# Performance work log

Measured on AMD Instinct MI355X. Metric: run time of the kernel, lower is better.

## Reference

```python
import jax, jax.numpy as jnp
import numpy as np

B, S, H, D, HID = 2, 4096, 16, 64, 1024
NUM_HASHES, CHUNK, NUM_BUCKETS = 2, 64, 128
N_BEFORE, N_AFTER = 1, 0
HASH_SEED = 0
SELF_MASK_VALUE = -1e5  # fp32 self-mask value from source buffers
EPS = 1e-6


def _look_adjacent(x, n_before, n_after):
    # x: [B,H,C,chunk,...]; concat chunks rolled along chunk axis (2) onto within-chunk axis (3)
    slices = [jnp.roll(x, -i, axis=2) for i in range(-n_before, n_after + 1)]
    return jnp.concatenate(slices, axis=3)


def _hash_vectors(vectors, rotations, num_buckets):
    # vectors: [B,H,S,D]; rotations: [H,D,NUM_HASHES,num_buckets//2] (shared q/k, seed reset in source)
    v = jax.lax.stop_gradient(vectors)  # vectors.detach() in source
    rotated = jnp.einsum('bhsd,hdnr->bhnsr', v, rotations)
    rotated = jnp.concatenate([rotated, -rotated], axis=-1)
    buckets = jnp.argmax(rotated, axis=-1)  # [B,H,NUM_HASHES,S]
    offsets = (jnp.arange(NUM_HASHES) * num_buckets).reshape(1, 1, -1, 1)
    return (buckets + offsets).reshape(vectors.shape[0], H, -1)  # [B,H,NUM_HASHES*S]


def _sorted_and_undo(buckets, seq_len):
    orig = jnp.arange(NUM_HASHES * seq_len) % seq_len
    scaled = seq_len * buckets + orig  # stable within-bucket ordering by position
    sorted_idx = jnp.argsort(scaled, axis=-1)
    undo_idx = jnp.argsort(sorted_idx, axis=-1)  # scatter-inverse of the sort
    return sorted_idx, undo_idx


def _len_and_dim_norm(x):
    var = jnp.mean(x * x, axis=-1, keepdims=True)
    return x * jax.lax.rsqrt(var + EPS) * np.float32(1.0 / np.sqrt(D))


def setup_inputs() -> dict:
    key = jax.random.key(0)
    k1, k2, k3, k4 = jax.random.split(key, 4)
    return {
        'decoder_states': jax.random.normal(k1, (B, S, HID), jnp.float32),
        'hidden_states': jax.random.normal(k2, (B, S, HID), jnp.float32),
        'w_qk': jax.random.normal(k3, (HID, H * D), jnp.float32) / np.float32(np.sqrt(HID)),
        'w_v': jax.random.normal(k4, (HID, H * D), jnp.float32) / np.float32(np.sqrt(HID)),
    }


def reference(decoder_states, hidden_states, w_qk, w_v):
    # projections (bias-free, Reformer-style), split heads -> [B,H,S,D]
    q = (decoder_states @ w_qk).reshape(B, S, H, D).transpose(0, 2, 1, 3)
    k = (hidden_states @ w_qk).reshape(B, S, H, D).transpose(0, 2, 1, 3)
    v = (hidden_states @ w_v).reshape(B, S, H, D).transpose(0, 2, 1, 3)

    rotations = jax.random.normal(jax.random.key(HASH_SEED),
                                  (H, D, NUM_HASHES, NUM_BUCKETS // 2), jnp.float32)
    q_buckets = _hash_vectors(q, rotations, NUM_BUCKETS)
    k_buckets = _hash_vectors(k, rotations, NUM_BUCKETS)
    sorted_q_idx, _ = _sorted_and_undo(q_buckets, S)
    sorted_k_idx, undo_k_idx = _sorted_and_undo(k_buckets, S)
    sorted_q_pos = sorted_q_idx % S
    sorted_k_pos = sorted_k_idx % S

    gather = lambda x, idx: jnp.take_along_axis(x, idx[..., None], axis=2)
    qs = gather(q, sorted_q_pos)  # [B,H,NUM_HASHES*S,D]
    ks = gather(k, sorted_k_pos)
    vs = gather(v, sorted_k_pos)

    n_chunks = NUM_HASHES * S // CHUNK
    to_chunks = lambda x: x.reshape(B, H, n_chunks, CHUNK, D)
    qs, ks, vs = to_chunks(qs), to_chunks(ks), to_chunks(vs)
    ks = _len_and_dim_norm(ks)

    ks = _look_adjacent(ks, N_BEFORE, N_AFTER)  # [B,H,C,2*CHUNK,D]
    vs = _look_adjacent(vs, N_BEFORE, N_AFTER)
    dots = jnp.einsum('bhcqd,bhckd->bhcqk', qs, ks)

    # self-mask: query position == adjacent key position (both from sorted QUERY idx, per source)
    q_idx = sorted_q_pos.reshape(B, H, n_chunks, CHUNK)
    kv_idx = _look_adjacent(q_idx, N_BEFORE, N_AFTER)  # [B,H,C,2*CHUNK]
    self_mask = q_idx[..., :, None] != kv_idx[..., None, :]
    dots = jnp.where(self_mask, dots, SELF_MASK_VALUE)

    logits = jax.nn.logsumexp(dots, axis=-1, keepdims=True)
    probs = jnp.exp(dots - logits)
    out = jnp.einsum('bhcqk,bhckd->bhcqd', probs, vs)

    out = out.reshape(B, H, NUM_HASHES * S, D)
    logits = logits.reshape(B, H, NUM_HASHES * S)
    # ReverseSort uses the KEY undo indices (as in source)
    out = jnp.take_along_axis(out, undo_k_idx[..., None], axis=2)
    logits = jnp.take_along_axis(logits, undo_k_idx, axis=2)

    # merge hash rounds via logsumexp weights (num_hashes > 1 branch)
    out = out.reshape(B, H, NUM_HASHES, S, D)
    logits = logits.reshape(B, H, NUM_HASHES, S, 1)
    w = jnp.exp(logits - jax.nn.logsumexp(logits, axis=2, keepdims=True))
    out = jnp.sum(out * w, axis=2)  # [B,H,S,D]
    return out.transpose(0, 2, 1, 3).reshape(B, S, H * D)
```

## Files before the change

kernel.cpp:

```cpp
#include <hip/hip_runtime.h>
#include <cstdint>
#include <cstddef>

#define BB 2
#define SS 4096
#define HH 16
#define DD 64
#define HID 1024
#define NHASH 2
#define CHUNK 64
#define NBUCK 128
#define NCHUNKS 128
#define NSORT 8192
#define BHN 32

#define KC_BLOCK 288

static constexpr size_t SZ_QKV  = (size_t)BB*HH*SS*DD*4;
static constexpr size_t OFF_Q   = 0;
static constexpr size_t OFF_K   = OFF_Q + SZ_QKV;
static constexpr size_t OFF_V   = OFF_K + SZ_QKV;
static constexpr size_t OFF_ROT = OFF_V + SZ_QKV;
static constexpr size_t OFF_QB  = OFF_ROT + (size_t)131072*4;
static constexpr size_t OFF_KB  = OFF_QB + (size_t)BHN*NSORT*4;
static constexpr size_t OFF_SQ  = OFF_KB + (size_t)BHN*NSORT*4;
static constexpr size_t OFF_SK  = OFF_SQ + (size_t)BHN*NSORT*4;
static constexpr size_t OFF_OUTR= OFF_SK + (size_t)BHN*NSORT*4;
static constexpr size_t OFF_LR  = OFF_OUTR + (size_t)BHN*NSORT*DD*4;
static constexpr size_t OFF_QBF = OFF_LR + (size_t)BHN*NSORT*4;
static constexpr size_t OFF_KBF = OFF_QBF + (size_t)BHN*SS*DD*2;
static constexpr size_t WS_REQUIRED = OFF_KBF + (size_t)BHN*SS*DD*2;

__device__ __forceinline__ float nofma_mul(float a, float b) {
  float r = a * b;
  asm("" : "+v"(r));
  return r;
}

__device__ __forceinline__ float xla_log1p_f32(float x) {
  float t = nofma_mul(-0.5f, x) + 1.0f;
  float small = nofma_mul(t, x);
  float onep = 1.0f + x;
  float big = (float)log((double)onep);
  return (fabsf(x) < 1e-4f) ? small : big;
}

__device__ __forceinline__ float erfinv_xla_f32(float x) {
  float nxx = -nofma_mul(x, x);
  float w = -xla_log1p_f32(nxx);
  float p;
  if (w < 5.0f) {
    float ww = w - 2.5f;
    p = 2.81022636e-08f;
    p = nofma_mul(p, ww) + 3.43273939e-07f;
    p = nofma_mul(p, ww) + -3.5233877e-06f;
    p = nofma_mul(p, ww) + -4.39150654e-06f;
    p = nofma_mul(p, ww) + 0.00021858087f;
    p = nofma_mul(p, ww) + -0.00125372503f;
    p = nofma_mul(p, ww) + -0.00417768164f;
    p = nofma_mul(p, ww) + 0.246640727f;
    p = nofma_mul(p, ww) + 1.50140941f;
  } else {
    float ww = sqrtf(w) - 3.0f;
    p = -0.000200214257f;
    p = nofma_mul(p, ww) + 0.000100950558f;
    p = nofma_mul(p, ww) + 0.00134934322f;
    p = nofma_mul(p, ww) + -0.00367342844f;
    p = nofma_mul(p, ww) + 0.00573950773f;
    p = nofma_mul(p, ww) + -0.0076224613f;
    p = nofma_mul(p, ww) + 0.00943887047f;
    p = nofma_mul(p, ww) + 1.00167406f;
    p = nofma_mul(p, ww) + 2.83297682f;
  }
  return nofma_mul(p, x);
}

__global__ void gen_rot_kernel(float* __restrict__ rot) {
  unsigned i = blockIdx.x * 256 + threadIdx.x;
  if (i >= 131072u) return;
  unsigned x0 = 0u, x1 = i;
  const unsigned ks2 = 0x1BD11BDAu;
#define TF_ROUND(r) { x0 += x1; x1 = (x1 << r) | (x1 >> (32 - r)); x1 ^= x0; }
  TF_ROUND(13) TF_ROUND(15) TF_ROUND(26) TF_ROUND(6)
              x1 += ks2 + 1u;
  TF_ROUND(17) TF_ROUND(29) TF_ROUND(16) TF_ROUND(24)
   x0 += ks2; x1 += 2u;
  TF_ROUND(13) TF_ROUND(15) TF_ROUND(26) TF_ROUND(6)
              x1 += 3u;
  TF_ROUND(17) TF_ROUND(29) TF_ROUND(16) TF_ROUND(24)
              x1 += ks2 + 4u;
  TF_ROUND(13) TF_ROUND(15) TF_ROUND(26) TF_ROUND(6)
   x0 += ks2; x1 += 5u;
#undef TF_ROUND
  unsigned bits = x0 ^ x1;
  float f = __uint_as_float(0x3f800000u | (bits >> 9)) - 1.0f;
  float u = f * 2.0f - 0.99999994f;
  u = fmaxf(-0.99999994f, u);
  rot[i] = nofma_mul(1.41421356f, erfinv_xla_f32(u));
}

__device__ __forceinline__ unsigned short f2bf(float f) {
  unsigned u = __float_as_uint(f);
  return (unsigned short)((u + 0x7fffu + ((u >> 16) & 1u)) >> 16);
}

__global__ __launch_bounds__(256) void gemm_kernel(const float* __restrict__ A,
                                                   const float* __restrict__ W,
                                                   float* __restrict__ dst,
                                                   unsigned short* __restrict__ dstb) {
  __shared__ float As[32][132];
  __shared__ float Bs[32][68];
  const int m0 = blockIdx.x * 128;
  const int n0 = blockIdx.y * 64;
  const int tid = threadIdx.x;
  const int tr = tid >> 4, tc = tid & 15;
  float accT[8][4], acc[8][4];
#pragma unroll
  for (int i = 0; i < 8; ++i)
#pragma unroll
    for (int j2 = 0; j2 < 4; ++j2) { accT[i][j2] = 0.f; acc[i][j2] = 0.f; }

  float4 av[4], bv[2];
#pragma unroll
  for (int it = 0; it < 4; ++it) {
    int id = tid + it * 256;
    av[it] = *(const float4*)(A + (size_t)(m0 + (id >> 3)) * 1024 + ((id & 7) << 2));
  }
#pragma unroll
  for (int it = 0; it < 2; ++it) {
    int id = tid + it * 256;
    bv[it] = *(const float4*)(W + (size_t)(id >> 4) * 1024 + n0 + ((id & 15) << 2));
  }
  for (int kk = 0; kk < 1024; kk += 32) {
#pragma unroll
    for (int it = 0; it < 4; ++it) {
      int id = tid + it * 256;
      int m = id >> 3, kq = (id & 7) << 2;
      As[kq + 0][m] = av[it].x;
      As[kq + 1][m] = av[it].y;
      As[kq + 2][m] = av[it].z;
      As[kq + 3][m] = av[it].w;
    }
#pragma unroll
    for (int it = 0; it < 2; ++it) {
      int id = tid + it * 256;
      *(float4*)&Bs[id >> 4][(id & 15) << 2] = bv[it];
    }
    __syncthreads();
    if (kk + 32 < 1024) {
      int kn = kk + 32;
#pragma unroll
      for (int it = 0; it < 4; ++it) {
        int id = tid + it * 256;
        av[it] = *(const float4*)(A + (size_t)(m0 + (id >> 3)) * 1024 + kn + ((id & 7) << 2));
      }
#pragma unroll
      for (int it = 0; it < 2; ++it) {
        int id = tid + it * 256;
        bv[it] = *(const float4*)(W + (size_t)(kn + (id >> 4)) * 1024 + n0 + ((id & 15) << 2));
      }
    }
#pragma unroll
    for (int k = 0; k < 32; ++k) {
      float4 a0 = *(const float4*)&As[k][tr * 8];
      float4 a1 = *(const float4*)&As[k][tr * 8 + 4];
      float4 b0 = *(const float4*)&Bs[k][tc * 4];
      float a[8] = {a0.x, a0.y, a0.z, a0.w, a1.x, a1.y, a1.z, a1.w};
      float b[4] = {b0.x, b0.y, b0.z, b0.w};
#pragma unroll
      for (int i = 0; i < 8; ++i)
#pragma unroll
        for (int j2 = 0; j2 < 4; ++j2)
          acc[i][j2] = fmaf(a[i], b[j2], acc[i][j2]);
    }
    __syncthreads();
    if (((kk + 32) % KC_BLOCK) == 0) {
#pragma unroll
      for (int i = 0; i < 8; ++i)
#pragma unroll
        for (int j2 = 0; j2 < 4; ++j2) { accT[i][j2] += acc[i][j2]; acc[i][j2] = 0.f; }
    }
  }
#pragma unroll
  for (int i = 0; i < 8; ++i)
#pragma unroll
    for (int j2 = 0; j2 < 4; ++j2) accT[i][j2] += acc[i][j2];

  const int h = n0 >> 6;
  const int d = tc << 2;
#pragma unroll
  for (int i = 0; i < 8; ++i) {
    int m = m0 + tr * 8 + i;
    int b = m >> 12, s = m & 4095;
    size_t base = (((size_t)(b * 16 + h) * 4096 + s) << 6) + d;
    float4 t = {accT[i][0], accT[i][1], accT[i][2], accT[i][3]};
    *(float4*)(dst + base) = t;
    ushort4 tb = {f2bf(t.x), f2bf(t.y), f2bf(t.z), f2bf(t.w)};
    *(ushort4*)(dstb + base) = tb;
  }
}

typedef __attribute__((ext_vector_type(8))) short bf16x8;
typedef __attribute__((ext_vector_type(4))) float f32x4;

__device__ __forceinline__ bf16x8 cvt8(float4 lo, float4 hi) {
  bf16x8 r;
  r[0] = (short)f2bf(lo.x); r[1] = (short)f2bf(lo.y);
  r[2] = (short)f2bf(lo.z); r[3] = (short)f2bf(lo.w);
  r[4] = (short)f2bf(hi.x); r[5] = (short)f2bf(hi.y);
  r[6] = (short)f2bf(hi.z); r[7] = (short)f2bf(hi.w);
  return r;
}

__global__ __launch_bounds__(256) void gemm_v_mfma(const float* __restrict__ Af,
                                                   const float* __restrict__ Wf,
                                                   unsigned short* __restrict__ dst) {
  __shared__ unsigned short Bt[64][40];
  const int m0 = blockIdx.x * 64;
  const int n0 = blockIdx.y * 64;
  const int tid = threadIdx.x;
  const int w = tid >> 6, l = tid & 63;
  f32x4 acc[4];
#pragma unroll
  for (int fi = 0; fi < 4; ++fi) acc[fi] = {0.f, 0.f, 0.f, 0.f};

  const int arow = m0 + w * 16 + (l & 15);
  const int kgrp = (l >> 4) * 8;
  for (int kk = 0; kk < 1024; kk += 32) {
    {
      int k = tid >> 3, n8 = (tid & 7) * 8;
      const float* wp = Wf + (size_t)(kk + k) * 1024 + n0 + n8;
      bf16x8 v = cvt8(*(const float4*)wp, *(const float4*)(wp + 4));
#pragma unroll
      for (int i = 0; i < 8; ++i) Bt[n8 + i][k] = (unsigned short)v[i];
    }
    __syncthreads();
    const float* ap = Af + (size_t)arow * 1024 + kk + kgrp;
    bf16x8 a = cvt8(*(const float4*)ap, *(const float4*)(ap + 4));
#pragma unroll
    for (int fi = 0; fi < 4; ++fi) {
      bf16x8 b = *(const bf16x8*)(&Bt[fi * 16 + (l & 15)][kgrp]);
      acc[fi] = __builtin_amdgcn_mfma_f32_16x16x32_bf16(a, b, acc[fi], 0, 0, 0);
    }
    __syncthreads();
  }
  const int h = n0 >> 6;
  const int mrow = m0 + w * 16 + (l >> 4) * 4;
#pragma unroll
  for (int fi = 0; fi < 4; ++fi) {
    int d = fi * 16 + (l & 15);
#pragma unroll
    for (int r = 0; r < 4; ++r) {
      int m = mrow + r;
      int b = m >> 12, s = m & 4095;
      dst[(((size_t)(b * 16 + h) * 4096 + s) << 6) + d] = f2bf(acc[fi][r]);
    }
  }
}

__global__ __launch_bounds__(128) void hash_kernel(const float* __restrict__ x,
                                                   const float* __restrict__ rot,
                                                   int* __restrict__ buck) {
  __shared__ float rs[8192];
  const int bh = blockIdx.y;
  const int h = bh & 15;
  const int s0 = blockIdx.x * 128;
  const int tid = threadIdx.x;
  for (int off = tid * 4; off < 8192; off += 512)
    *(float4*)&rs[off] = *(const float4*)(rot + (size_t)h * 8192 + off);
  __syncthreads();
  const int s = s0 + tid;
  const float* xr = x + ((size_t)bh * SS + s) * DD;
  float xv[64];
#pragma unroll
  for (int d4 = 0; d4 < 16; ++d4) {
    float4 t = *(const float4*)(xr + d4 * 4);
    xv[d4 * 4] = t.x; xv[d4 * 4 + 1] = t.y; xv[d4 * 4 + 2] = t.z; xv[d4 * 4 + 3] = t.w;
  }
#pragma unroll
  for (int n = 0; n < 2; ++n) {
    float acc[64];
#pragma unroll
    for (int r = 0; r < 64; ++r) acc[r] = 0.f;
#pragma unroll 2
    for (int d4 = 0; d4 < 16; ++d4) {
#pragma unroll
      for (int dd = 0; dd < 4; ++dd) {
        const float xd = xv[d4 * 4 + dd];
        const float* rp = rs + (d4 * 4 + dd) * 128 + n * 64;
#pragma unroll
        for (int r4 = 0; r4 < 16; ++r4) {
          float4 rv = *(const float4*)(rp + r4 * 4);
          acc[r4 * 4 + 0] = fmaf(xd, rv.x, acc[r4 * 4 + 0]);
          acc[r4 * 4 + 1] = fmaf(xd, rv.y, acc[r4 * 4 + 1]);
          acc[r4 * 4 + 2] = fmaf(xd, rv.z, acc[r4 * 4 + 2]);
          acc[r4 * 4 + 3] = fmaf(xd, rv.w, acc[r4 * 4 + 3]);
        }
      }
    }
    float best = -3.402823466e38f;
    int bi = 0;
#pragma unroll
    for (int idx = 0; idx < 128; ++idx) {
      float val = (idx < 64) ? acc[idx] : -acc[idx - 64];
      if (val > best) { best = val; bi = idx; }
    }
    buck[(size_t)bh * NSORT + n * SS + s] = bi + n * NBUCK;
  }
}

__global__ __launch_bounds__(256) void sort_kernel(const int* __restrict__ buck,
                                                   int* __restrict__ sorted,
                                                   int* __restrict__ undo) {
  const int bh = blockIdx.x >> 1;
  const int half = blockIdx.x & 1;
  const int* bk = buck + (size_t)bh * NSORT + half * SS;
  int* out = sorted + (size_t)bh * NSORT + half * SS;
  int* und = undo + (size_t)bh * NSORT;
  __shared__ int cnt[64][128];
  __shared__ int bl[SS];
  __shared__ int bbase[128];
  __shared__ int total[128];
  const int tid = threadIdx.x;
  for (int i = tid; i < 64 * 128; i += 256) (&cnt[0][0])[i] = 0;
  __syncthreads();
#pragma unroll
  for (int j = 0; j < 16; ++j) {
    int i = j * 256 + tid;
    int e = bk[i];
    bl[i] = e;
    atomicAdd(&cnt[i >> 6][e & 127], 1);
  }
  __syncthreads();
  if (tid < 128) {
    int s = 0;
#pragma unroll 4
    for (int c = 0; c < 64; ++c) {
      int t = cnt[c][tid];
      cnt[c][tid] = s;
      s += t;
    }
    total[tid] = s;
  }
  __syncthreads();
  if (tid == 0) {
    int s = 0;
#pragma unroll 4
    for (int v = 0; v < 128; ++v) { bbase[v] = s; s += total[v]; }
  }
  __syncthreads();
  if (tid < 64) {
    const int i0 = tid << 6;
    const int orig0 = half * SS + i0;
#pragma unroll 4
    for (int j = 0; j < 64; ++j) {
      int v = bl[i0 + j] & 127;
      int off = cnt[tid][v];
      cnt[tid][v] = off + 1;
      int pos = bbase[v] + off;
      out[pos] = orig0 + j;
      und[orig0 + j] = half * SS + pos;
    }
  }
}

__global__ __launch_bounds__(256) void attn_mfma_kernel(
    const unsigned short* __restrict__ qb16, const unsigned short* __restrict__ kb16,
    const unsigned short* __restrict__ vb16,
    const int* __restrict__ sq, const int* __restrict__ sk,
    float* __restrict__ outr, float* __restrict__ lr) {
  const int c = blockIdx.x, bh = blockIdx.y;
  const int cprev = (c + NCHUNKS - 1) & (NCHUNKS - 1);
  __shared__ unsigned short Qs[64][80];
  __shared__ unsigned short Ks[128][80];
  __shared__ unsigned short Vt[64][136];
  __shared__ unsigned short Ps[64][136];
  __shared__ int qpos[64];
  __shared__ int kvpos[128];
  __shared__ int krow[128];
  __shared__ float kscale[128];
  const int tid = threadIdx.x;
  const int* sqb = sq + (size_t)bh * NSORT;
  const int* skb = sk + (size_t)bh * NSORT;
  if (tid < 64) {
    int sqc = sqb[c * 64 + tid];
    int sqp = sqb[cprev * 64 + tid];
    qpos[tid] = sqc & (SS - 1);
    kvpos[tid] = sqp & (SS - 1);
    kvpos[64 + tid] = sqc & (SS - 1);
    krow[tid] = skb[cprev * 64 + tid] & (SS - 1);
    krow[64 + tid] = skb[c * 64 + tid] & (SS - 1);
  }
  __syncthreads();
  const unsigned short* kbase = kb16 + (size_t)bh * SS * DD;
  const unsigned short* vbase = vb16 + (size_t)bh * SS * DD;
  const unsigned short* qbase = qb16 + (size_t)bh * SS * DD;
#pragma unroll
  for (int it = 0; it < 4; ++it) {
    int id = tid + it * 256;
    int row = id >> 3, seg = id & 7;
    *(bf16x8*)&Ks[row][seg * 8] = *(const bf16x8*)(kbase + (size_t)krow[row] * DD + seg * 8);
  }
#pragma unroll
  for (int it = 0; it < 2; ++it) {
    int id = tid + it * 256;
    int row = id >> 3, seg = id & 7;
    *(bf16x8*)&Qs[row][seg * 8] = *(const bf16x8*)(qbase + (size_t)qpos[row] * DD + seg * 8);
  }
#pragma unroll
  for (int it = 0; it < 4; ++it) {
    int id = tid + it * 256;
    int col = id & 127, dg = id >> 7;
    bf16x8 v = *(const bf16x8*)(vbase + (size_t)krow[col] * DD + dg * 8);
#pragma unroll
    for (int i = 0; i < 8; ++i) Vt[dg * 8 + i][col] = (unsigned short)v[i];
  }
  __syncthreads();
  if (tid < 128) {
    float ss = 0.f;
#pragma unroll
    for (int seg = 0; seg < 8; ++seg) {
      bf16x8 t = *(const bf16x8*)&Ks[tid][seg * 8];
#pragma unroll
      for (int i = 0; i < 8; ++i) {
        float f = __uint_as_float(((unsigned)(unsigned short)t[i]) << 16);
        ss = fmaf(f, f, ss);
      }
    }
    kscale[tid] = rsqrtf(ss * (1.f / 64.f) + 1e-6f) * 0.125f;
  }
  __syncthreads();

  const int w = tid >> 6, l = tid & 63;
  const int lc = l & 15, lg = l >> 4;
  bf16x8 a0 = *(const bf16x8*)&Qs[w * 16 + lc][lg * 8];
  bf16x8 a1 = *(const bf16x8*)&Qs[w * 16 + lc][32 + lg * 8];
  f32x4 accs[8];
#pragma unroll
  for (int fi = 0; fi < 8; ++fi) {
    f32x4 acc = {0.f, 0.f, 0.f, 0.f};
    bf16x8 b0 = *(const bf16x8*)&Ks[fi * 16 + lc][lg * 8];
    bf16x8 b1 = *(const bf16x8*)&Ks[fi * 16 + lc][32 + lg * 8];
    acc = __builtin_amdgcn_mfma_f32_16x16x32_bf16(a0, b0, acc, 0, 0, 0);
    acc = __builtin_amdgcn_mfma_f32_16x16x32_bf16(a1, b1, acc, 0, 0, 0);
    accs[fi] = acc;
  }
  float kcs[8]; int kvp[8];
#pragma unroll
  for (int fi = 0; fi < 8; ++fi) { kcs[fi] = kscale[fi * 16 + lc]; kvp[fi] = kvpos[fi * 16 + lc]; }
  float ex[8][4], logit_r[4], seinv_r[4];
#pragma unroll
  for (int r = 0; r < 4; ++r) {
    const int qp = qpos[w * 16 + lg * 4 + r];
    float mr = -3.402823466e38f;
#pragma unroll
    for (int fi = 0; fi < 8; ++fi) {
      float d = accs[fi][r] * kcs[fi];
      if (qp == kvp[fi]) d = -1e5f;
      ex[fi][r] = d;
      mr = fmaxf(mr, d);
    }
    mr = fmaxf(mr, __shfl_xor(mr, 1));
    mr = fmaxf(mr, __shfl_xor(mr, 2));
    mr = fmaxf(mr, __shfl_xor(mr, 4));
    mr = fmaxf(mr, __shfl_xor(mr, 8));
    float s = 0.f;
#pragma unroll
    for (int fi = 0; fi < 8; ++fi) { float e = expf(ex[fi][r] - mr); ex[fi][r] = e; s += e; }
    s += __shfl_xor(s, 1);
    s += __shfl_xor(s, 2);
    s += __shfl_xor(s, 4);
    s += __shfl_xor(s, 8);
    logit_r[r] = mr + logf(s);
    seinv_r[r] = 1.f / s;
  }
#pragma unroll
  for (int r = 0; r < 4; ++r) {
    int row = w * 16 + lg * 4 + r;
#pragma unroll
    for (int fi = 0; fi < 8; ++fi)
      Ps[row][fi * 16 + lc] = f2bf(ex[fi][r]);
    if (lc == 0) lr[(size_t)bh * NSORT + c * 64 + row] = logit_r[r];
  }
  __syncthreads();
  f32x4 acco[4];
#pragma unroll
  for (int fi2 = 0; fi2 < 4; ++fi2) acco[fi2] = {0.f, 0.f, 0.f, 0.f};
#pragma unroll
  for (int kg = 0; kg < 4; ++kg) {
    bf16x8 a = *(const bf16x8*)&Ps[w * 16 + lc][kg * 32 + lg * 8];
#pragma unroll
    for (int fi2 = 0; fi2 < 4; ++fi2) {
      bf16x8 b = *(const bf16x8*)&Vt[fi2 * 16 + lc][kg * 32 + lg * 8];
      acco[fi2] = __builtin_amdgcn_mfma_f32_16x16x32_bf16(a, b, acco[fi2], 0, 0, 0);
    }
  }
#pragma unroll
  for (int fi2 = 0; fi2 < 4; ++fi2) {
    int d = fi2 * 16 + lc;
#pragma unroll
    for (int r = 0; r < 4; ++r) {
      int row = w * 16 + lg * 4 + r;
      outr[((size_t)bh * NSORT + c * 64 + row) * DD + d] = acco[fi2][r] * seinv_r[r];
    }
  }
}

__global__ void merge_kernel(const float* __restrict__ outr, const float* __restrict__ lr,
                             const int* __restrict__ undo, float* __restrict__ out) {
  const int idx = blockIdx.x * 256 + threadIdx.x;
  const int d4 = idx & 15;
  const int s = (idx >> 4) & (SS - 1);
  const int bh = idx >> 16;
  const int b = bh >> 4, h = bh & 15;
  const int u0 = undo[(size_t)bh * NSORT + s];
  const int u1 = undo[(size_t)bh * NSORT + SS + s];
  const float l0 = lr[(size_t)bh * NSORT + u0];
  const float l1 = lr[(size_t)bh * NSORT + u1];
  const float m = fmaxf(l0, l1);
  float w0 = expf(l0 - m), w1 = expf(l1 - m);
  const float inv = 1.f / (w0 + w1);
  w0 *= inv; w1 *= inv;
  const float4 r0 = *(const float4*)(outr + ((size_t)bh * NSORT + u0) * DD + d4 * 4);
  const float4 r1 = *(const float4*)(outr + ((size_t)bh * NSORT + u1) * DD + d4 * 4);
  float4 o;
  o.x = w0 * r0.x + w1 * r1.x;
  o.y = w0 * r0.y + w1 * r1.y;
  o.z = w0 * r0.z + w1 * r1.z;
  o.w = w0 * r0.w + w1 * r1.w;
  *(float4*)(out + ((size_t)(b * SS + s) * 1024) + h * 64 + d4 * 4) = o;
}

extern "C" void kernel_launch(void* const* d_in, const int* in_sizes, int n_in,
                              void* d_out, int out_size, void* d_ws, size_t ws_size,
                              hipStream_t stream) {
  if (ws_size < WS_REQUIRED) return;
  const float* dec = (const float*)d_in[0];
  const float* hid = (const float*)d_in[1];
  const float* wqk = (const float*)d_in[2];
  const float* wv  = (const float*)d_in[3];
  float* out = (float*)d_out;
  char* ws = (char*)d_ws;
  float* q    = (float*)(ws + OFF_Q);
  float* kk   = (float*)(ws + OFF_K);
  unsigned short* vbf = (unsigned short*)(ws + OFF_V);
  float* rotp = (float*)(ws + OFF_ROT);
  int*   qb   = (int*)(ws + OFF_QB);
  int*   kbk  = (int*)(ws + OFF_KB);
  int*   sqi  = (int*)(ws + OFF_SQ);
  int*   ski  = (int*)(ws + OFF_SK);
  float* outr = (float*)(ws + OFF_OUTR);
  float* lrp  = (float*)(ws + OFF_LR);
  unsigned short* qbf = (unsigned short*)(ws + OFF_QBF);
  unsigned short* kbf = (unsigned short*)(ws + OFF_KBF);

  gen_rot_kernel<<<512, 256, 0, stream>>>(rotp);
  gemm_kernel<<<dim3(64, 16), 256, 0, stream>>>(dec, wqk, q, qbf);
  gemm_kernel<<<dim3(64, 16), 256, 0, stream>>>(hid, wqk, kk, kbf);
  gemm_v_mfma<<<dim3(128, 16), 256, 0, stream>>>(hid, wv, vbf);
  hash_kernel<<<dim3(32, 32), 128, 0, stream>>>(q, rotp, qb);
  hash_kernel<<<dim3(32, 32), 128, 0, stream>>>(kk, rotp, kbk);
  sort_kernel<<<64, 256, 0, stream>>>(qb, sqi, qb);
  sort_kernel<<<64, 256, 0, stream>>>(kbk, ski, kbk);
  attn_mfma_kernel<<<dim3(128, 32), 256, 0, stream>>>(qbf, kbf, vbf, sqi, ski, outr, lrp);
  merge_kernel<<<8192, 256, 0, stream>>>(outr, lrp, kbk, out);
}
```

Measured before the change: 801.9 us.

## Merge Q/K projection GEMMs into one launch with larger tiles and split-K passes

Combines the separate Q and K fp32 projection GEMMs into a single kernel whose grid covers both inputs. The output tile per thread grows from 8x4 to 8x8 (128x128 block tiles) to raise FMA reuse per shared-memory load. The 288-wide partial-sum blocking that was done in registers is replaced by four sequential launches over K chunks that accumulate through global memory, which keeps the same summation order. The bf16 copy is written only on the last pass. This adds extra global read/write traffic for the partial sums and more launches, and the larger tile raises register pressure.

```diff
diff --git a/kernel.cpp b/kernel.cpp
--- a/kernel.cpp
+++ b/kernel.cpp
@@ -14,7 +14,6 @@
 #define NSORT 8192
 #define BHN 32
 
-#define KC_BLOCK 288
 
 static constexpr size_t SZ_QKV  = (size_t)BB*HH*SS*DD*4;
 static constexpr size_t OFF_Q   = 0;
@@ -104,34 +103,39 @@
   return (unsigned short)((u + 0x7fffu + ((u >> 16) & 1u)) >> 16);
 }
 
-__global__ __launch_bounds__(256) void gemm_kernel(const float* __restrict__ A,
-                                                   const float* __restrict__ W,
-                                                   float* __restrict__ dst,
-                                                   unsigned short* __restrict__ dstb) {
+__global__ __launch_bounds__(256) void gemm_kc(const float* __restrict__ dec,
+                                               const float* __restrict__ hid,
+                                               const float* __restrict__ W,
+                                               float* __restrict__ qd,
+                                               float* __restrict__ kd,
+                                               unsigned short* __restrict__ qbf,
+                                               unsigned short* __restrict__ kbf,
+                                               int kstart, int nk, int accum, int wb) {
   __shared__ float As[32][132];
-  __shared__ float Bs[32][68];
-  const int m0 = blockIdx.x * 128;
-  const int n0 = blockIdx.y * 64;
+  __shared__ float Bs[32][132];
+  int m0 = blockIdx.x * 128;
+  const float* A;
+  float* dst;
+  unsigned short* dstb;
+  if (m0 < 8192) { A = dec; dst = qd; dstb = qbf; }
+  else           { A = hid; dst = kd; dstb = kbf; m0 -= 8192; }
+  const int n0 = blockIdx.y * 128;
   const int tid = threadIdx.x;
   const int tr = tid >> 4, tc = tid & 15;
-  float accT[8][4], acc[8][4];
+  float acc[8][8];
 #pragma unroll
   for (int i = 0; i < 8; ++i)
 #pragma unroll
-    for (int j2 = 0; j2 < 4; ++j2) { accT[i][j2] = 0.f; acc[i][j2] = 0.f; }
-
-  float4 av[4], bv[2];
+    for (int j = 0; j < 8; ++j) acc[i][j] = 0.f;
+
+  float4 av[4], bv[4];
 #pragma unroll
   for (int it = 0; it < 4; ++it) {
     int id = tid + it * 256;
-    av[it] = *(const float4*)(A + (size_t)(m0 + (id >> 3)) * 1024 + ((id & 7) << 2));
-  }
-#pragma unroll
-  for (int it = 0; it < 2; ++it) {
-    int id = tid + it * 256;
-    bv[it] = *(const float4*)(W + (size_t)(id >> 4) * 1024 + n0 + ((id & 15) << 2));
-  }
-  for (int kk = 0; kk < 1024; kk += 32) {
+    av[it] = *(const float4*)(A + (size_t)(m0 + (id >> 3)) * 1024 + kstart + ((id & 7) << 2));
+    bv[it] = *(const float4*)(W + (size_t)(kstart + (id >> 5)) * 1024 + n0 + ((id & 31) << 2));
+  }
+  for (int t = 0; t < nk; ++t) {
 #pragma unroll
     for (int it = 0; it < 4; ++it) {
       int id = tid + it * 256;
@@ -140,63 +144,54 @@
       As[kq + 1][m] = av[it].y;
       As[kq + 2][m] = av[it].z;
       As[kq + 3][m] = av[it].w;
-    }
-#pragma unroll
-    for (int it = 0; it < 2; ++it) {
-      int id = tid + it * 256;
-      *(float4*)&Bs[id >> 4][(id & 15) << 2] = bv[it];
+      *(float4*)&Bs[id >> 5][(id & 31) << 2] = bv[it];
     }
     __syncthreads();
-    if (kk + 32 < 1024) {
-      int kn = kk + 32;
+    if (t + 1 < nk) {
+      int kn = kstart + (t + 1) * 32;
 #pragma unroll
       for (int it = 0; it < 4; ++it) {
         int id = tid + it * 256;
         av[it] = *(const float4*)(A + (size_t)(m0 + (id >> 3)) * 1024 + kn + ((id & 7) << 2));
-      }
-#pragma unroll
-      for (int it = 0; it < 2; ++it) {
-        int id = tid + it * 256;
-        bv[it] = *(const float4*)(W + (size_t)(kn + (id >> 4)) * 1024 + n0 + ((id & 15) << 2));
+        bv[it] = *(const float4*)(W + (size_t)(kn + (id >> 5)) * 1024 + n0 + ((id & 31) << 2));
       }
     }
 #pragma unroll
     for (int k = 0; k < 32; ++k) {
       float4 a0 = *(const float4*)&As[k][tr * 8];
       float4 a1 = *(const float4*)&As[k][tr * 8 + 4];
-      float4 b0 = *(const float4*)&Bs[k][tc * 4];
+      float4 b0 = *(const float4*)&Bs[k][tc * 8];
+      float4 b1 = *(const float4*)&Bs[k][tc * 8 + 4];
       float a[8] = {a0.x, a0.y, a0.z, a0.w, a1.x, a1.y, a1.z, a1.w};
-      float b[4] = {b0.x, b0.y, b0.z, b0.w};
+      float b[8] = {b0.x, b0.y, b0.z, b0.w, b1.x, b1.y, b1.z, b1.w};
 #pragma unroll
       for (int i = 0; i < 8; ++i)
 #pragma unroll
-        for (int j2 = 0; j2 < 4; ++j2)
-          acc[i][j2] = fmaf(a[i], b[j2], acc[i][j2]);
+        for (int j = 0; j < 8; ++j)
+          acc[i][j] = fmaf(a[i], b[j], acc[i][j]);
     }
     __syncthreads();
-    if (((kk + 32) % KC_BLOCK) == 0) {
-#pragma unroll
-      for (int i = 0; i < 8; ++i)
-#pragma unroll
-        for (int j2 = 0; j2 < 4; ++j2) { accT[i][j2] += acc[i][j2]; acc[i][j2] = 0.f; }
-    }
-  }
-#pragma unroll
-  for (int i = 0; i < 8; ++i)
-#pragma unroll
-    for (int j2 = 0; j2 < 4; ++j2) accT[i][j2] += acc[i][j2];
-
-  const int h = n0 >> 6;
-  const int d = tc << 2;
+  }
 #pragma unroll
   for (int i = 0; i < 8; ++i) {
     int m = m0 + tr * 8 + i;
     int b = m >> 12, s = m & 4095;
-    size_t base = (((size_t)(b * 16 + h) * 4096 + s) << 6) + d;
-    float4 t = {accT[i][0], accT[i][1], accT[i][2], accT[i][3]};
-    *(float4*)(dst + base) = t;
-    ushort4 tb = {f2bf(t.x), f2bf(t.y), f2bf(t.z), f2bf(t.w)};
-    *(ushort4*)(dstb + base) = tb;
+#pragma unroll
+    for (int jq = 0; jq < 2; ++jq) {
+      int col = n0 + tc * 8 + jq * 4;
+      int h = col >> 6, d = col & 63;
+      size_t base = (((size_t)(b * 16 + h) * 4096 + s) << 6) + d;
+      float4 t = {acc[i][jq * 4], acc[i][jq * 4 + 1], acc[i][jq * 4 + 2], acc[i][jq * 4 + 3]};
+      if (accum) {
+        float4 o = *(const float4*)(dst + base);
+        t.x += o.x; t.y += o.y; t.z += o.z; t.w += o.w;
+      }
+      *(float4*)(dst + base) = t;
+      if (wb) {
+        ushort4 tb = {f2bf(t.x), f2bf(t.y), f2bf(t.z), f2bf(t.w)};
+        *(ushort4*)(dstb + base) = tb;
+      }
+    }
   }
 }
 
@@ -555,8 +550,12 @@
   unsigned short* kbf = (unsigned short*)(ws + OFF_KBF);
 
   gen_rot_kernel<<<512, 256, 0, stream>>>(rotp);
-  gemm_kernel<<<dim3(64, 16), 256, 0, stream>>>(dec, wqk, q, qbf);
-  gemm_kernel<<<dim3(64, 16), 256, 0, stream>>>(hid, wqk, kk, kbf);
+  const int kst[4] = {0, 288, 576, 864};
+  const int nks[4] = {9, 9, 9, 5};
+  for (int cc = 0; cc < 4; ++cc)
+    gemm_kc<<<dim3(128, 8), 256, 0, stream>>>(dec, hid, wqk, q, kk, qbf, kbf,
+                                              kst[cc], nks[cc], cc > 0 ? 1 : 0,
+                                              cc == 3 ? 1 : 0);
   gemm_v_mfma<<<dim3(128, 16), 256, 0, stream>>>(hid, wv, vbf);
   hash_kernel<<<dim3(32, 32), 128, 0, stream>>>(q, rotp, qb);
   hash_kernel<<<dim3(32, 32), 128, 0, stream>>>(kk, rotp, kbk);
```

Result: slower. 876.1 us (+9.3%).
